# Optimization experiments

Hardware: AMD Instinct MI355X
Metric: run time of the kernel (lower is better)

The kernel has to match this reference:

```python
import jax, jax.numpy as jnp
import numpy as np
from jax.scipy.special import gammaln

BIG_NEG = -1e9
MAX_K = 32


def setup_inputs() -> dict:
    key = jax.random.key(0)
    k1, k2, k3, k4, k5, k6 = jax.random.split(key, 6)
    b, N1, d, C1 = 4, 512, 64, 32
    features = jax.random.normal(k1, (b, N1, d), dtype=jnp.float32)
    lengths = jax.random.randint(k2, (b,), N1 // 2, N1 + 1)
    gaussian_means = 0.1 * jax.random.normal(k3, (C1, d), dtype=jnp.float32)
    gaussian_cov = jnp.eye(d, dtype=jnp.float32)  # requires_grad=False in torch, identity init
    poisson_log_rates = jax.random.uniform(k4, (C1,), jnp.float32, 0.5, 3.0)
    transition_logits = 0.1 * jax.random.normal(k5, (C1, C1), dtype=jnp.float32)
    init_logits = jax.random.uniform(k6, (C1,), jnp.float32, 0.0, 1.0)
    return {
        "features": features,
        "lengths": lengths,
        "gaussian_means": gaussian_means,
        "gaussian_cov": gaussian_cov,
        "poisson_log_rates": poisson_log_rates,
        "transition_logits": transition_logits,
        "init_logits": init_logits,
    }


def _score_features(features, lengths, gaussian_means, gaussian_cov,
                    poisson_log_rates, transition_logits, init_logits):
    b, N1, d = features.shape
    C1 = gaussian_means.shape[0]
    K = min(MAX_K, N1)
    C = C1 + 1        # EOS-augmented class count
    N = N1 + 1        # EOS-augmented sequence length

    # --- initial_log_probs ---
    init = jax.nn.log_softmax(init_logits, axis=0)

    # --- transition_log_probs: mask self-transitions, log_softmax over dim 0 ---
    eye = jnp.eye(C1, dtype=bool)
    trans = jax.nn.log_softmax(jnp.where(eye, BIG_NEG, transition_logits), axis=0)

    # --- emission_log_probs: shared full-covariance Gaussian per class ---
    L = jnp.linalg.cholesky(gaussian_cov)
    logdet = 2.0 * jnp.sum(jnp.log(jnp.diag(L)))
    Minv = jax.scipy.linalg.cho_solve((L, True), jnp.eye(d, dtype=gaussian_cov.dtype))
    diff = features[:, :, None, :] - gaussian_means[None, None, :, :]   # (b, N1, C1, d)
    maha = jnp.einsum('bncd,de,bnce->bnc', diff, Minv, diff)             # (b, N1, C1)
    em = -0.5 * (maha + d * jnp.log(2.0 * jnp.pi) + logdet)              # (b, N1, C1)

    # --- length_log_probs: Poisson over k = 0..K-1 ---
    ks = jnp.arange(K, dtype=features.dtype)
    len_scores = (ks[:, None] * poisson_log_rates[None, :]
                  - jnp.exp(poisson_log_rates)[None, :]
                  - gammaln(ks + 1.0)[:, None])                          # (K, C1)

    # --- EOS augmentation (add_eos=True) ---
    trans_aug = jnp.full((C, C), BIG_NEG, dtype=features.dtype)
    trans_aug = trans_aug.at[:C1, :C1].set(trans).at[C1, :].set(0.0)
    init_aug = jnp.full((C,), BIG_NEG, dtype=features.dtype).at[:C1].set(init)
    len_aug = jnp.full((K, C), BIG_NEG, dtype=features.dtype)
    len_aug = len_aug.at[:, :C1].set(len_scores).at[1, C1].set(0.0)

    # emission_augmented (b, N, C): valid frames keep em, EOS column is 0 at any
    # position t that equals some instance's length (faithful to the torch loop,
    # which writes emission_augmented[:, length, C1] = 0 for ALL batch rows).
    t = jnp.arange(N)
    valid = t[None, :N1] < lengths[:, None]                              # (b, N1)
    main = jnp.where(valid[:, :, None], em, BIG_NEG)                     # (b, N1, C1)
    main = jnp.concatenate([main, jnp.full((b, 1, C1), BIG_NEG, dtype=features.dtype)], axis=1)  # (b, N, C1)
    is_len = jnp.any(t[None, :] == lengths[:, None], axis=0)             # (N,)
    eos_col = jnp.where(is_len, 0.0, BIG_NEG).astype(features.dtype)     # (N,)
    em_aug = jnp.concatenate([main, jnp.broadcast_to(eos_col[None, :, None], (b, N, 1))], axis=2)  # (b, N, C)

    # --- sliding window sums over all k at once via cumulative sums ---
    # sliding_sum(x, k)[t] = sum_{j=0..k-1} x[t+j] with zero padding past N
    csum = jnp.concatenate([jnp.zeros((b, 1, C), dtype=features.dtype),
                            jnp.cumsum(em_aug, axis=1)], axis=1)          # (b, N+1, C)
    t_idx = jnp.arange(N - 1)                                            # = N1 positions
    k_idx = jnp.arange(K)
    end = jnp.clip(t_idx[:, None] + k_idx[None, :], 0, N)                # (N1, K)
    wins = csum[:, end, :] - csum[:, t_idx, None, :]                     # (b, N1, K, C); k=0 slice is 0 (not added in torch either)

    # --- assemble edge scores: b x (N-1) x K x C x C ---
    scores = (trans_aug[None, None, None, :, :]
              + len_aug[None, None, :, None, :]
              + wins[:, :, :, None, :])
    scores = scores.at[:, 0].add(init_aug)  # broadcasts over last axis
    # final-frame correction: scores[:, N-1-k, k, :, :] += em_aug[:, N-1].view(b, C, 1), k >= 1
    mask = (t_idx[:, None] + k_idx[None, :] == N - 1) & (k_idx[None, :] >= 1)   # (N1, K)
    em_last = em_aug[:, N - 1]                                           # (b, C)
    scores = scores + jnp.where(mask[None, :, :, None, None],
                                em_last[:, None, None, :, None], 0.0)
    return scores


def reference(features, lengths, gaussian_means, gaussian_cov,
              poisson_log_rates, transition_logits, init_logits):
    return _score_features(features, lengths, gaussian_means, gaussian_cov,
                           poisson_log_rates, transition_logits, init_logits)
```

## Files before the change

kernel.cpp:

```cpp
#include <hip/hip_runtime.h>
#include <hip/hip_bf16.h>
#include <math.h>

#define BIGNEG (-1000000000.0f)

constexpr int OFF_MINV   = 0;
constexpr int OFF_LOGDET = 4096;
constexpr int OFF_Q      = 4100;
constexpr int OFF_S      = 6148;
constexpr int OFF_TRANS  = 6180;
constexpr int OFF_LENAUG = 7269;
constexpr int OFF_INITA  = 8325;
constexpr int OFF_EOS    = 8358;
constexpr int OFF_EMLAST = 8871;
constexpr int OFF_EMT    = 8904;
constexpr int OFF_CSUM   = 74440;

__global__ __launch_bounds__(256) void setup_kernel(
    const float* __restrict__ cov, const float* __restrict__ means,
    const float* __restrict__ plr, const float* __restrict__ tlogits,
    const float* __restrict__ ilogits, const int* __restrict__ lengths,
    float* __restrict__ ws)
{
    __shared__ float A[64][130];
    __shared__ float rd[64];
    __shared__ float lg[64];
    __shared__ float lse_t[32];
    __shared__ float ilse;
    const int tid = threadIdx.x;

    for (int idx = tid; idx < 64 * 64; idx += 256) {
        const int r = idx >> 6, c = idx & 63;
        A[r][c] = cov[idx];
        A[r][64 + c] = (r == c) ? 1.f : 0.f;
    }
    __syncthreads();

    const int r = tid >> 2;
    const int g = tid & 3;
    for (int p = 0; p < 64; ++p) {
        const float d = A[p][p];
        const float f = (r == p) ? 0.f : A[r][p] / d;
        #pragma unroll
        for (int i = 0; i < 32; ++i) {
            const int c = g + (i << 2);
            A[r][c] = fmaf(-f, A[p][c], A[r][c]);
        }
        __syncthreads();
    }
    if (tid < 64) {
        const float d = A[tid][tid];
        rd[tid] = 1.f / d;
        lg[tid] = logf(d);
    }
    __syncthreads();
    if (tid == 0) {
        float ld = 0.f;
        for (int j = 0; j < 64; ++j) ld += lg[j];
        ws[OFF_LOGDET] = ld;
    }

    for (int idx = tid; idx < 4096; idx += 256) {
        const int row = idx >> 6;
        ws[OFF_MINV + idx] = A[row][64 + (idx & 63)] * rd[row];
    }
    for (int idx = tid; idx < 32 * 64; idx += 256) {
        const int c = idx >> 6, t = idx & 63;
        float acc = 0.f;
        for (int e = 0; e < 64; ++e) acc += A[t][64 + e] * means[c * 64 + e];
        ws[OFF_Q + c * 64 + t] = acc * rd[t];
    }
    __syncthreads();
    if (tid < 32) {
        const int c = tid;
        float acc = 0.f;
        for (int t = 0; t < 64; ++t) acc += means[c * 64 + t] * ws[OFF_Q + c * 64 + t];
        ws[OFF_S + c] = acc;
    }
    if (tid < 32) {
        const int j = tid;
        float mx = -INFINITY;
        for (int i = 0; i < 32; ++i) {
            const float x = (i == j) ? BIGNEG : tlogits[i * 32 + j];
            mx = fmaxf(mx, x);
        }
        float sum = 0.f;
        for (int i = 0; i < 32; ++i) {
            const float x = (i == j) ? BIGNEG : tlogits[i * 32 + j];
            sum += expf(x - mx);
        }
        lse_t[j] = mx + logf(sum);
    }
    if (tid == 0) {
        float mx = -INFINITY;
        for (int i = 0; i < 32; ++i) mx = fmaxf(mx, ilogits[i]);
        float sum = 0.f;
        for (int i = 0; i < 32; ++i) sum += expf(ilogits[i] - mx);
        ilse = mx + logf(sum);
    }
    __syncthreads();
    for (int idx = tid; idx < 1089; idx += 256) {
        const int i = idx / 33, j = idx - i * 33;
        float v;
        if (i == 32) v = 0.f;
        else if (j == 32) v = BIGNEG;
        else if (i == j) v = BIGNEG - lse_t[j];
        else v = tlogits[i * 32 + j] - lse_t[j];
        ws[OFF_TRANS + idx] = v;
    }
    if (tid < 33) ws[OFF_INITA + tid] = (tid < 32) ? (ilogits[tid] - ilse) : BIGNEG;
    for (int idx = tid; idx < 32 * 33; idx += 256) {
        const int k = idx / 33, j = idx - k * 33;
        float v;
        if (j < 32) v = (float)k * plr[j] - expf(plr[j]) - lgammaf((float)k + 1.f);
        else        v = (k == 1) ? 0.f : BIGNEG;
        ws[OFF_LENAUG + idx] = v;
    }
    const int l0 = lengths[0], l1 = lengths[1], l2 = lengths[2], l3 = lengths[3];
    for (int t = tid; t < 513; t += 256) {
        const bool any = (l0 == t) | (l1 == t) | (l2 == t) | (l3 == t);
        ws[OFF_EOS + t] = any ? 0.f : BIGNEG;
    }
    if (tid < 33) {
        float v = BIGNEG;
        if (tid == 32) {
            const bool any = (l0 == 512) | (l1 == 512) | (l2 == 512) | (l3 == 512);
            v = any ? 0.f : BIGNEG;
        }
        ws[OFF_EMLAST + tid] = v;
    }
}

__global__ __launch_bounds__(256) void em_kernel(
    const float* __restrict__ features, float* __restrict__ ws)
{
    __shared__ float sM[64][65];
    __shared__ float sq[32][65];
    __shared__ float sf[4][64];
    __shared__ float ss[32];
    const int tid = threadIdx.x;
    for (int idx = tid; idx < 4096; idx += 256) sM[idx >> 6][idx & 63] = ws[OFF_MINV + idx];
    for (int idx = tid; idx < 2048; idx += 256) sq[idx >> 6][idx & 63] = ws[OFF_Q + idx];
    if (tid < 32) ss[tid] = ws[OFF_S + tid];
    const float logdet = ws[OFF_LOGDET];
    const int w = tid >> 6, lane = tid & 63;
    const int p = blockIdx.x * 4 + w;
    sf[w][lane] = features[p * 64 + lane];
    __syncthreads();

    float u = 0.f;
    for (int e = 0; e < 64; ++e) u += sM[lane][e] * sf[w][e];
    float a = sf[w][lane] * u;
    for (int m = 32; m >= 1; m >>= 1) a += __shfl_xor(a, m, 64);

    const int c = lane >> 1, h = lane & 1;
    float pd = 0.f;
    const int eb = h * 32;
    for (int e = 0; e < 32; ++e) pd += sf[w][eb + e] * sq[c][eb + e];
    pd += __shfl_xor(pd, 1, 64);

    const float em = -0.5f * (a - 2.f * pd + ss[c] + 64.f * 1.8378770664093453f + logdet);
    const int b = p >> 9, n = p & 511;
    if (h == 0) ws[OFF_EMT + (b * 32 + c) * 512 + n] = em;
}

__global__ __launch_bounds__(64) void csum_kernel(
    const int* __restrict__ lengths, float* __restrict__ ws)
{
    const int blk = blockIdx.x;
    const int b = blk / 33, c = blk - b * 33;
    const int lane = threadIdx.x;
    const int len = lengths[b];
    const float* emt = ws + OFF_EMT + (b * 32 + c) * 512;
    const float* eos = ws + OFF_EOS;
    const int t0 = lane * 9;
    float v[9];
#pragma unroll
    for (int i = 0; i < 9; ++i) {
        const int t = t0 + i;
        float x = 0.f;
        if (t <= 512) {
            if (c == 32)      x = eos[t];
            else if (t < 512 && t < len) x = emt[t];
            else              x = BIGNEG;
        }
        v[i] = x;
    }
#pragma unroll
    for (int i = 1; i < 9; ++i) v[i] += v[i - 1];
    const float tot = v[8];
    float inc = tot;
    for (int off = 1; off < 64; off <<= 1) {
        const float y = __shfl_up(inc, off, 64);
        if (lane >= off) inc += y;
    }
    const float excl = inc - tot;
    float* cs = ws + OFF_CSUM + b * 514 * 33 + c;
    if (lane == 0) cs[0] = 0.f;
#pragma unroll
    for (int i = 0; i < 9; ++i) {
        const int t = t0 + i;
        if (t <= 512) cs[(t + 1) * 33] = excl + v[i];
    }
}

__global__ __launch_bounds__(256) void score_kernel(
    const float* __restrict__ ws, float* __restrict__ out)
{
    __shared__ float sT[1089];
    __shared__ float sA[32 * 33];
    const int tid = threadIdx.x;
    const int blk = blockIdx.x;
    const int b = blk >> 9, t = blk & 511;
    const float* trans  = ws + OFF_TRANS;
    const float* lenaug = ws + OFF_LENAUG;
    const float* inita  = ws + OFF_INITA;
    const float* emlast = ws + OFF_EMLAST;
    const float* cs     = ws + OFF_CSUM + b * 514 * 33;

    for (int idx = tid; idx < 1089; idx += 256) sT[idx] = trans[idx];
    for (int idx = tid; idx < 1056; idx += 256) {
        const int k = idx / 33, j = idx - k * 33;
        int end = t + k; if (end > 513) end = 513;
        float v = cs[end * 33 + j] - cs[t * 33 + j] + lenaug[idx];
        if (t == 0) v += inita[j];
        sA[idx] = v;
    }
    __syncthreads();

    float tv[5], el[5];
    int jj[5];
#pragma unroll
    for (int m = 0; m < 5; ++m) {
        const int idx = tid + 256 * m;
        if (idx < 1089) {
            const int i = idx / 33;
            jj[m] = idx - i * 33;
            tv[m] = sT[idx];
            el[m] = emlast[i];
        } else { jj[m] = 0; tv[m] = 0.f; el[m] = 0.f; }
    }
    const bool has5 = (tid < 65);
    const int kk = 512 - t;
    float* ob = out + (size_t)(b * 512 + t) * 32 * 1089;
    for (int k = 0; k < 32; ++k) {
        const float add = (k == kk) ? 1.f : 0.f;
        const float* Ak = sA + k * 33;
        float* op = ob + (size_t)k * 1089;
#pragma unroll
        for (int m = 0; m < 4; ++m)
            __builtin_nontemporal_store(tv[m] + Ak[jj[m]] + add * el[m], op + tid + 256 * m);
        if (has5)
            __builtin_nontemporal_store(tv[4] + Ak[jj[4]] + add * el[4], op + tid + 1024);
    }
}

extern "C" void kernel_launch(void* const* d_in, const int* in_sizes, int n_in,
                              void* d_out, int out_size, void* d_ws, size_t ws_size,
                              hipStream_t stream) {
    (void)in_sizes; (void)n_in; (void)out_size; (void)ws_size;
    const float* features = (const float*)d_in[0];
    const int*   lengths  = (const int*)d_in[1];
    const float* means    = (const float*)d_in[2];
    const float* cov      = (const float*)d_in[3];
    const float* plr      = (const float*)d_in[4];
    const float* tlog     = (const float*)d_in[5];
    const float* ilog     = (const float*)d_in[6];
    float* ws  = (float*)d_ws;
    float* out = (float*)d_out;

    setup_kernel<<<1, 256, 0, stream>>>(cov, means, plr, tlog, ilog, lengths, ws);
    em_kernel<<<512, 256, 0, stream>>>(features, ws);
    csum_kernel<<<132, 64, 0, stream>>>(lengths, ws);
    score_kernel<<<2048, 256, 0, stream>>>(ws, out);
}
```

Before: 475.1 us.

## Fuse window cumsum into score kernel and do Gauss-Jordan inversion in registers

Removes the separate csum kernel. Each score block now computes its own 31-step running sum of emissions starting at frame t, which drops one launch and the round trip of the cumsum buffer through global memory. The setup kernel's 64x64 matrix inversion moves from a shared-memory Gauss-Jordan with 64 block barriers to a single wavefront that keeps rows in registers and broadcasts pivot rows with readlane. The cost is redundant per-block summation work and heavy register use in setup, while the score kernel stays bound by its large output stores.

```diff
diff --git a/kernel.cpp b/kernel.cpp
--- a/kernel.cpp
+++ b/kernel.cpp
@@ -1,5 +1,4 @@
 #include <hip/hip_runtime.h>
-#include <hip/hip_bf16.h>
 #include <math.h>
 
 #define BIGNEG (-1000000000.0f)
@@ -14,7 +13,10 @@
 constexpr int OFF_EOS    = 8358;
 constexpr int OFF_EMLAST = 8871;
 constexpr int OFF_EMT    = 8904;
-constexpr int OFF_CSUM   = 74440;
+
+__device__ __forceinline__ float rl(float x, int l) {
+    return __int_as_float(__builtin_amdgcn_readlane(__float_as_int(x), l));
+}
 
 __global__ __launch_bounds__(256) void setup_kernel(
     const float* __restrict__ cov, const float* __restrict__ means,
@@ -22,53 +24,61 @@
     const float* __restrict__ ilogits, const int* __restrict__ lengths,
     float* __restrict__ ws)
 {
-    __shared__ float A[64][130];
-    __shared__ float rd[64];
-    __shared__ float lg[64];
+    __shared__ float A[64][65];
     __shared__ float lse_t[32];
     __shared__ float ilse;
     const int tid = threadIdx.x;
 
-    for (int idx = tid; idx < 64 * 64; idx += 256) {
-        const int r = idx >> 6, c = idx & 63;
-        A[r][c] = cov[idx];
-        A[r][64 + c] = (r == c) ? 1.f : 0.f;
-    }
-    __syncthreads();
-
-    const int r = tid >> 2;
-    const int g = tid & 3;
-    for (int p = 0; p < 64; ++p) {
-        const float d = A[p][p];
-        const float f = (r == p) ? 0.f : A[r][p] / d;
-        #pragma unroll
-        for (int i = 0; i < 32; ++i) {
-            const int c = g + (i << 2);
-            A[r][c] = fmaf(-f, A[p][c], A[r][c]);
-        }
-        __syncthreads();
-    }
+    for (int idx = tid; idx < 64 * 64; idx += 256)
+        A[idx >> 6][idx & 63] = cov[idx];
+    __syncthreads();
+
     if (tid < 64) {
-        const float d = A[tid][tid];
-        rd[tid] = 1.f / d;
-        lg[tid] = logf(d);
-    }
-    __syncthreads();
-    if (tid == 0) {
-        float ld = 0.f;
-        for (int j = 0; j < 64; ++j) ld += lg[j];
-        ws[OFF_LOGDET] = ld;
-    }
-
-    for (int idx = tid; idx < 4096; idx += 256) {
-        const int row = idx >> 6;
-        ws[OFF_MINV + idx] = A[row][64 + (idx & 63)] * rd[row];
-    }
+        const int lane = tid;
+        float L[64], R[64];
+#pragma unroll
+        for (int c = 0; c < 64; ++c) {
+            L[c] = A[lane][c];
+            R[c] = (lane == c) ? 1.f : 0.f;
+        }
+        float curcol = L[0];
+        float myd = 1.f;
+#pragma unroll 1
+        for (int p = 0; p < 64; ++p) {
+            const float d = rl(curcol, p);
+            const float invd = 1.f / d;
+            const float f = (lane == p) ? 0.f : curcol * invd;
+            myd = (lane == p) ? d : myd;
+            float nextcol = 0.f;
+#pragma unroll
+            for (int c = 0; c < 64; ++c) {
+                const float piv = rl(L[c], p);
+                L[c] = fmaf(-f, piv, L[c]);
+                if (c == p + 1) nextcol = L[c];
+            }
+#pragma unroll
+            for (int c = 0; c < 64; ++c) {
+                const float piv = rl(R[c], p);
+                R[c] = fmaf(-f, piv, R[c]);
+            }
+            curcol = nextcol;
+        }
+        const float rdv = 1.f / myd;
+#pragma unroll
+        for (int c = 0; c < 64; ++c) A[lane][c] = R[c] * rdv;
+        float lg = logf(myd);
+        for (int m = 32; m >= 1; m >>= 1) lg += __shfl_xor(lg, m, 64);
+        if (lane == 0) ws[OFF_LOGDET] = lg;
+    }
+    __syncthreads();
+
+    for (int idx = tid; idx < 4096; idx += 256)
+        ws[OFF_MINV + idx] = A[idx >> 6][idx & 63];
     for (int idx = tid; idx < 32 * 64; idx += 256) {
         const int c = idx >> 6, t = idx & 63;
         float acc = 0.f;
-        for (int e = 0; e < 64; ++e) acc += A[t][64 + e] * means[c * 64 + e];
-        ws[OFF_Q + c * 64 + t] = acc * rd[t];
+        for (int e = 0; e < 64; ++e) acc += A[t][e] * means[c * 64 + e];
+        ws[OFF_Q + idx] = acc;
     }
     __syncthreads();
     if (tid < 32) {
@@ -164,72 +174,49 @@
     if (h == 0) ws[OFF_EMT + (b * 32 + c) * 512 + n] = em;
 }
 
-__global__ __launch_bounds__(64) void csum_kernel(
-    const int* __restrict__ lengths, float* __restrict__ ws)
-{
-    const int blk = blockIdx.x;
-    const int b = blk / 33, c = blk - b * 33;
-    const int lane = threadIdx.x;
-    const int len = lengths[b];
-    const float* emt = ws + OFF_EMT + (b * 32 + c) * 512;
-    const float* eos = ws + OFF_EOS;
-    const int t0 = lane * 9;
-    float v[9];
-#pragma unroll
-    for (int i = 0; i < 9; ++i) {
-        const int t = t0 + i;
-        float x = 0.f;
-        if (t <= 512) {
-            if (c == 32)      x = eos[t];
-            else if (t < 512 && t < len) x = emt[t];
-            else              x = BIGNEG;
-        }
-        v[i] = x;
-    }
-#pragma unroll
-    for (int i = 1; i < 9; ++i) v[i] += v[i - 1];
-    const float tot = v[8];
-    float inc = tot;
-    for (int off = 1; off < 64; off <<= 1) {
-        const float y = __shfl_up(inc, off, 64);
-        if (lane >= off) inc += y;
-    }
-    const float excl = inc - tot;
-    float* cs = ws + OFF_CSUM + b * 514 * 33 + c;
-    if (lane == 0) cs[0] = 0.f;
-#pragma unroll
-    for (int i = 0; i < 9; ++i) {
-        const int t = t0 + i;
-        if (t <= 512) cs[(t + 1) * 33] = excl + v[i];
-    }
-}
-
 __global__ __launch_bounds__(256) void score_kernel(
-    const float* __restrict__ ws, float* __restrict__ out)
+    const float* __restrict__ ws, const int* __restrict__ lengths,
+    float* __restrict__ out)
 {
     __shared__ float sT[1089];
     __shared__ float sA[32 * 33];
     const int tid = threadIdx.x;
     const int blk = blockIdx.x;
     const int b = blk >> 9, t = blk & 511;
-    const float* trans  = ws + OFF_TRANS;
-    const float* lenaug = ws + OFF_LENAUG;
-    const float* inita  = ws + OFF_INITA;
-    const float* emlast = ws + OFF_EMLAST;
-    const float* cs     = ws + OFF_CSUM + b * 514 * 33;
-
-    for (int idx = tid; idx < 1089; idx += 256) sT[idx] = trans[idx];
+
+    for (int idx = tid; idx < 1089; idx += 256) sT[idx] = ws[OFF_TRANS + idx];
+    const bool t0 = (t == 0);
     for (int idx = tid; idx < 1056; idx += 256) {
-        const int k = idx / 33, j = idx - k * 33;
-        int end = t + k; if (end > 513) end = 513;
-        float v = cs[end * 33 + j] - cs[t * 33 + j] + lenaug[idx];
-        if (t == 0) v += inita[j];
+        const int j = idx % 33;
+        float v = ws[OFF_LENAUG + idx];
+        if (t0) v += ws[OFF_INITA + j];
         sA[idx] = v;
     }
     __syncthreads();
+
+    if (tid < 33) {
+        const int j = tid;
+        const int len = lengths[b];
+        const float* emc = ws + OFF_EMT + (b * 32 + j) * 512;
+        const float* eos = ws + OFF_EOS;
+        float vals[31];
+#pragma unroll
+        for (int i = 0; i < 31; ++i) {
+            const int u = t + i;
+            float x;
+            if (u > 512)      x = 0.f;
+            else if (j == 32) x = eos[u];
+            else              x = (u < len) ? emc[u] : BIGNEG;
+            vals[i] = x;
+        }
+        float run = 0.f;
+#pragma unroll
+        for (int k = 1; k < 32; ++k) { run += vals[k - 1]; sA[k * 33 + j] += run; }
+    }
 
     float tv[5], el[5];
     int jj[5];
+    const float* emlast = ws + OFF_EMLAST;
 #pragma unroll
     for (int m = 0; m < 5; ++m) {
         const int idx = tid + 256 * m;
@@ -240,6 +227,8 @@
             el[m] = emlast[i];
         } else { jj[m] = 0; tv[m] = 0.f; el[m] = 0.f; }
     }
+    __syncthreads();
+
     const bool has5 = (tid < 65);
     const int kk = 512 - t;
     float* ob = out + (size_t)(b * 512 + t) * 32 * 1089;
@@ -271,6 +260,5 @@
 
     setup_kernel<<<1, 256, 0, stream>>>(cov, means, plr, tlog, ilog, lengths, ws);
     em_kernel<<<512, 256, 0, stream>>>(features, ws);
-    csum_kernel<<<132, 64, 0, stream>>>(lengths, ws);
-    score_kernel<<<2048, 256, 0, stream>>>(ws, out);
-}
+    score_kernel<<<2048, 256, 0, stream>>>(ws, lengths, out);
+}
```

Result: slower. 491.4 us (+3.4%).

## Invert covariance in registers with one wavefront and coalesce emission stores

Applied to the files above, without the earlier changes.

The Gauss-Jordan inversion in the setup kernel moves from a 256-thread shared-memory loop with a block barrier per pivot to a single 64-lane wavefront. Each lane holds one row of the matrix and its inverse in registers, and pivot-row values are broadcast with readlane. This removes 64 barriers and most shared-memory traffic, but leaves 192 threads idle during the inversion and raises register pressure with 128 floats per lane. The emission kernel now stages results in shared memory so the strided global stores become four consecutive positions per class.

```diff
diff --git a/kernel.cpp b/kernel.cpp
--- a/kernel.cpp
+++ b/kernel.cpp
@@ -1,5 +1,4 @@
 #include <hip/hip_runtime.h>
-#include <hip/hip_bf16.h>
 #include <math.h>
 
 #define BIGNEG (-1000000000.0f)
@@ -16,59 +15,71 @@
 constexpr int OFF_EMT    = 8904;
 constexpr int OFF_CSUM   = 74440;
 
+__device__ __forceinline__ float rl(float x, int l) {
+    return __int_as_float(__builtin_amdgcn_readlane(__float_as_int(x), l));
+}
+
 __global__ __launch_bounds__(256) void setup_kernel(
     const float* __restrict__ cov, const float* __restrict__ means,
     const float* __restrict__ plr, const float* __restrict__ tlogits,
     const float* __restrict__ ilogits, const int* __restrict__ lengths,
     float* __restrict__ ws)
 {
-    __shared__ float A[64][130];
-    __shared__ float rd[64];
-    __shared__ float lg[64];
+    __shared__ float A[64][65];
     __shared__ float lse_t[32];
     __shared__ float ilse;
     const int tid = threadIdx.x;
 
-    for (int idx = tid; idx < 64 * 64; idx += 256) {
-        const int r = idx >> 6, c = idx & 63;
-        A[r][c] = cov[idx];
-        A[r][64 + c] = (r == c) ? 1.f : 0.f;
-    }
-    __syncthreads();
-
-    const int r = tid >> 2;
-    const int g = tid & 3;
-    for (int p = 0; p < 64; ++p) {
-        const float d = A[p][p];
-        const float f = (r == p) ? 0.f : A[r][p] / d;
-        #pragma unroll
-        for (int i = 0; i < 32; ++i) {
-            const int c = g + (i << 2);
-            A[r][c] = fmaf(-f, A[p][c], A[r][c]);
-        }
-        __syncthreads();
-    }
+    for (int idx = tid; idx < 64 * 64; idx += 256)
+        A[idx >> 6][idx & 63] = cov[idx];
+    __syncthreads();
+
     if (tid < 64) {
-        const float d = A[tid][tid];
-        rd[tid] = 1.f / d;
-        lg[tid] = logf(d);
-    }
-    __syncthreads();
-    if (tid == 0) {
-        float ld = 0.f;
-        for (int j = 0; j < 64; ++j) ld += lg[j];
-        ws[OFF_LOGDET] = ld;
-    }
-
-    for (int idx = tid; idx < 4096; idx += 256) {
-        const int row = idx >> 6;
-        ws[OFF_MINV + idx] = A[row][64 + (idx & 63)] * rd[row];
-    }
+        const int lane = tid;
+        float L[64], R[64];
+#pragma unroll
+        for (int c = 0; c < 64; ++c) {
+            L[c] = A[lane][c];
+            R[c] = (lane == c) ? 1.f : 0.f;
+        }
+        float curcol = L[0];
+        float myd = 1.f;
+#pragma unroll 1
+        for (int p = 0; p < 64; ++p) {
+            const float d = rl(curcol, p);
+            const float invd = 1.f / d;
+            const float f = (lane == p) ? 0.f : curcol * invd;
+            myd = (lane == p) ? d : myd;
+            float nextcol = 0.f;
+#pragma unroll
+            for (int c = 0; c < 64; ++c) {
+                const float piv = rl(L[c], p);
+                L[c] = fmaf(-f, piv, L[c]);
+                if (c == p + 1) nextcol = L[c];
+            }
+#pragma unroll
+            for (int c = 0; c < 64; ++c) {
+                const float piv = rl(R[c], p);
+                R[c] = fmaf(-f, piv, R[c]);
+            }
+            curcol = nextcol;
+        }
+        const float rdv = 1.f / myd;
+#pragma unroll
+        for (int c = 0; c < 64; ++c) A[lane][c] = R[c] * rdv;
+        float lg = logf(myd);
+        for (int m = 32; m >= 1; m >>= 1) lg += __shfl_xor(lg, m, 64);
+        if (lane == 0) ws[OFF_LOGDET] = lg;
+    }
+    __syncthreads();
+
+    for (int idx = tid; idx < 4096; idx += 256)
+        ws[OFF_MINV + idx] = A[idx >> 6][idx & 63];
     for (int idx = tid; idx < 32 * 64; idx += 256) {
         const int c = idx >> 6, t = idx & 63;
         float acc = 0.f;
-        for (int e = 0; e < 64; ++e) acc += A[t][64 + e] * means[c * 64 + e];
-        ws[OFF_Q + c * 64 + t] = acc * rd[t];
+        for (int e = 0; e < 64; ++e) acc += A[t][e] * means[c * 64 + e];
+        ws[OFF_Q + idx] = acc;
     }
     __syncthreads();
     if (tid < 32) {
@@ -138,6 +149,7 @@
     __shared__ float sq[32][65];
     __shared__ float sf[4][64];
     __shared__ float ss[32];
+    __shared__ float se[4][32];
     const int tid = threadIdx.x;
     for (int idx = tid; idx < 4096; idx += 256) sM[idx >> 6][idx & 63] = ws[OFF_MINV + idx];
     for (int idx = tid; idx < 2048; idx += 256) sq[idx >> 6][idx & 63] = ws[OFF_Q + idx];
@@ -160,8 +172,15 @@
     pd += __shfl_xor(pd, 1, 64);
 
     const float em = -0.5f * (a - 2.f * pd + ss[c] + 64.f * 1.8378770664093453f + logdet);
-    const int b = p >> 9, n = p & 511;
-    if (h == 0) ws[OFF_EMT + (b * 32 + c) * 512 + n] = em;
+    if (h == 0) se[w][c] = em;
+    __syncthreads();
+
+    if (tid < 128) {
+        const int cc = tid >> 2, wv = tid & 3;
+        const int p0 = blockIdx.x * 4;
+        const int b = p0 >> 9, n0 = p0 & 511;
+        ws[OFF_EMT + (b * 32 + cc) * 512 + n0 + wv] = se[wv][cc];
+    }
 }
 
 __global__ __launch_bounds__(64) void csum_kernel(
```

Result: slower. 493.5 us (+3.9%).

## Block Gauss-Jordan elimination in setup kernel with 4x4 pivot blocks

Applied to the files above, without the earlier changes.

Replaces the 64-step scalar Gauss-Jordan inversion in the single-block setup kernel with a 16-step blocked version. Each step inverts a 4x4 pivot block on one thread and applies a rank-4 update to all rows using float2 shared-memory accesses. This cuts the number of serialized barrier-separated steps by a factor of four. In exchange it adds a single-thread serial section per block and a different floating-point operation order, with no pivoting.

```diff
diff --git a/kernel.cpp b/kernel.cpp
--- a/kernel.cpp
+++ b/kernel.cpp
@@ -1,5 +1,4 @@
 #include <hip/hip_runtime.h>
-#include <hip/hip_bf16.h>
 #include <math.h>
 
 #define BIGNEG (-1000000000.0f)
@@ -23,8 +22,10 @@
     float* __restrict__ ws)
 {
     __shared__ float A[64][130];
+    __shared__ float Brows[4][130];
+    __shared__ float sBinv[4][4];
     __shared__ float rd[64];
-    __shared__ float lg[64];
+    __shared__ float lgacc;
     __shared__ float lse_t[32];
     __shared__ float ilse;
     const int tid = threadIdx.x;
@@ -34,31 +35,89 @@
         A[r][c] = cov[idx];
         A[r][64 + c] = (r == c) ? 1.f : 0.f;
     }
+    if (tid == 0) lgacc = 0.f;
     __syncthreads();
 
     const int r = tid >> 2;
     const int g = tid & 3;
-    for (int p = 0; p < 64; ++p) {
-        const float d = A[p][p];
-        const float f = (r == p) ? 0.f : A[r][p] / d;
-        #pragma unroll
-        for (int i = 0; i < 32; ++i) {
-            const int c = g + (i << 2);
-            A[r][c] = fmaf(-f, A[p][c], A[r][c]);
+    const int r4 = tid >> 6;
+    const int cc = tid & 63;
+
+    for (int blk = 0; blk < 16; ++blk) {
+        const int p0 = blk * 4;
+        Brows[r4][cc]      = A[p0 + r4][cc];
+        Brows[r4][cc + 64] = A[p0 + r4][cc + 64];
+        if (cc < 2) Brows[r4][cc + 128] = A[p0 + r4][cc + 128];
+        if (tid == 0) {
+            float B[4][4], V[4][4];
+#pragma unroll
+            for (int k = 0; k < 4; ++k)
+#pragma unroll
+                for (int m = 0; m < 4; ++m) {
+                    B[k][m] = A[p0 + k][p0 + m];
+                    V[k][m] = (k == m) ? 1.f : 0.f;
+                }
+            float ld = 0.f;
+#pragma unroll
+            for (int k = 0; k < 4; ++k) {
+                const float d = B[k][k];
+                ld += logf(d);
+                const float invd = 1.f / d;
+#pragma unroll
+                for (int rr = 0; rr < 4; ++rr) {
+                    if (rr == k) continue;
+                    const float f = B[rr][k] * invd;
+#pragma unroll
+                    for (int m = 0; m < 4; ++m) {
+                        B[rr][m] = fmaf(-f, B[k][m], B[rr][m]);
+                        V[rr][m] = fmaf(-f, V[k][m], V[rr][m]);
+                    }
+                }
+            }
+#pragma unroll
+            for (int k = 0; k < 4; ++k) {
+                const float s = 1.f / B[k][k];
+#pragma unroll
+                for (int m = 0; m < 4; ++m) sBinv[k][m] = V[k][m] * s;
+            }
+            lgacc += ld;
+#pragma unroll
+            for (int k = 0; k < 4; ++k) rd[p0 + k] = sBinv[k][k];
         }
         __syncthreads();
-    }
-    if (tid < 64) {
-        const float d = A[tid][tid];
-        rd[tid] = 1.f / d;
-        lg[tid] = logf(d);
-    }
-    __syncthreads();
-    if (tid == 0) {
-        float ld = 0.f;
-        for (int j = 0; j < 64; ++j) ld += lg[j];
-        ws[OFF_LOGDET] = ld;
-    }
+
+        float c0, c1, c2, c3;
+        if (r >= p0 && r < p0 + 4) {
+            const int k = r - p0;
+            const float ibkk = 1.f / sBinv[k][k];
+            c0 = (k == 0) ? 0.f : -sBinv[k][0] * ibkk;
+            c1 = (k == 1) ? 0.f : -sBinv[k][1] * ibkk;
+            c2 = (k == 2) ? 0.f : -sBinv[k][2] * ibkk;
+            c3 = (k == 3) ? 0.f : -sBinv[k][3] * ibkk;
+        } else {
+            const float a0 = A[r][p0 + 0], a1 = A[r][p0 + 1];
+            const float a2 = A[r][p0 + 2], a3 = A[r][p0 + 3];
+            c0 = a0 * sBinv[0][0] + a1 * sBinv[1][0] + a2 * sBinv[2][0] + a3 * sBinv[3][0];
+            c1 = a0 * sBinv[0][1] + a1 * sBinv[1][1] + a2 * sBinv[2][1] + a3 * sBinv[3][1];
+            c2 = a0 * sBinv[0][2] + a1 * sBinv[1][2] + a2 * sBinv[2][2] + a3 * sBinv[3][2];
+            c3 = a0 * sBinv[0][3] + a1 * sBinv[1][3] + a2 * sBinv[2][3] + a3 * sBinv[3][3];
+        }
+        float2* pa = reinterpret_cast<float2*>(&A[r][0]);
+        const float2* pb0 = reinterpret_cast<const float2*>(&Brows[0][0]);
+        const float2* pb1 = reinterpret_cast<const float2*>(&Brows[1][0]);
+        const float2* pb2 = reinterpret_cast<const float2*>(&Brows[2][0]);
+        const float2* pb3 = reinterpret_cast<const float2*>(&Brows[3][0]);
+        for (int u = g; u < 65; u += 4) {
+            float2 v = pa[u];
+            const float2 b0 = pb0[u], b1 = pb1[u], b2 = pb2[u], b3 = pb3[u];
+            v.x -= c0 * b0.x + c1 * b1.x + c2 * b2.x + c3 * b3.x;
+            v.y -= c0 * b0.y + c1 * b1.y + c2 * b2.y + c3 * b3.y;
+            pa[u] = v;
+        }
+        __syncthreads();
+    }
+
+    if (tid == 0) ws[OFF_LOGDET] = lgacc;
 
     for (int idx = tid; idx < 4096; idx += 256) {
         const int row = idx >> 6;
```

Result: faster. 441.3 us (-7.1%).
